# Performance work log

Hardware: AMD Instinct MI355X
Metric: run time of the kernel (lower is better)

Reference implementation:

```python
import jax, jax.numpy as jnp
import numpy as np


def setup_inputs() -> dict:
    key = jax.random.key(0)
    ks = jax.random.split(key, 6)
    T, F, INPUT_SIZE = 32768, 758, 730  # F = input_size + attributes(27) + 1(catch_ID)
    return {
        "x": jax.random.normal(ks[0], (T, F), dtype=jnp.float32),
        "weight_input": jax.random.normal(ks[1], (4, INPUT_SIZE), dtype=jnp.float32) * 0.05,
        "weight_recur": jax.random.normal(ks[2], (4, 1), dtype=jnp.float32) * 0.05,
        "bias": jax.random.normal(ks[3], (4, 1), dtype=jnp.float32) * 0.05,
        "reg_w": jax.random.normal(ks[4], (1, 1), dtype=jnp.float32),
        "reg_b": jax.random.normal(ks[5], (1,), dtype=jnp.float32),
        "h0": jnp.zeros((1,), dtype=jnp.float32),
        "c0": jnp.zeros((1,), dtype=jnp.float32),
    }


def reference(x, weight_input, weight_recur, bias, reg_w, reg_b, h0, c0):
    input_size = weight_input.shape[1]
    # x[:, :-attributes-1] in the original == first input_size columns
    x_feat = x[:, :input_size]                      # [T, input_size]
    # hoist the per-step mm(weight_input, x_t) into one GEMM: [T, 4]
    xp = x_feat @ weight_input.T
    wr = weight_recur[:, 0]                         # [4]
    b = bias[:, 0]                                  # [4]

    def step(carry, xp_t):
        h, c = carry                                # scalars (state_size == 1)
        gates = b + wr * h + xp_t                   # [4]
        f = jax.nn.sigmoid(gates[0])
        i = jax.nn.sigmoid(gates[1])
        o = jax.nn.sigmoid(gates[2])
        g = jnp.tanh(gates[3])
        c1 = f * c + i * g
        h1 = o * jnp.tanh(c1)
        return (h1, c1), (h1, c1)

    (_, _), (hs, cs) = jax.lax.scan(step, (h0[0], c0[0]), xp)
    h_n = jnp.concatenate([h0[None, :], hs[:, None]], axis=0)  # [T+1, 1]
    c_n = jnp.concatenate([c0[None, :], cs[:, None]], axis=0)  # [T+1, 1]
    q_t = (h_n @ reg_w.T + reg_b)[1:]                          # [T, 1]
    return q_t, h_n, c_n
```

## Files before the change

### kernel.cpp

```cpp
#include <hip/hip_runtime.h>

#define T_LEN 32768
#define F_DIM 758
#define IN_SZ 730
#define CHUNK_L 8
#define WARM_W 48
#define N_CHUNK (T_LEN / CHUNK_L)
#define SCAN_BLOCKS (N_CHUNK / 64)
#define STAGE_ROWS 560

#define GEMV_BLOCKS 512
#define GEMV_WAVES (GEMV_BLOCKS * 4)
#define ROWS_PER_WAVE (T_LEN / GEMV_WAVES)

__global__ __launch_bounds__(256) void gemv_gates(
    const float* __restrict__ x, const float* __restrict__ w,
    const float* __restrict__ bias, float* __restrict__ xpw) {
  const float L2E = 1.4426950408889634f;
  int lane = threadIdx.x & 63;
  int g    = lane & 3;
  int p    = lane >> 2;
  int wid  = (blockIdx.x * 256 + threadIdx.x) >> 6;

  const float* wg = w + (size_t)g * IN_SZ;
  float4 wv[12];
#pragma unroll
  for (int j = 0; j < 12; j++) {
    int c = p + 16 * j;
#pragma unroll
    for (int e = 0; e < 4; e++) {
      int k = 4 * c + e;
      ((float*)&wv[j])[e] = (k < IN_SZ) ? wg[k] : 0.f;
    }
  }
  float bg = bias[g];
  float cg = (g == 3) ? (-2.f * L2E) : (-L2E);

  const float4 z4 = {0.f, 0.f, 0.f, 0.f};
  float4 xa[12], xb[12];
  float res[ROWS_PER_WAVE];

  auto loadrow = [&](float4* dst, int row) {
    const float* xr = x + (size_t)row * F_DIM;
#pragma unroll
    for (int j = 0; j < 12; j++) {
      int c = p + 16 * j;
      dst[j] = (c < 183) ? *(const float4*)(xr + 4 * c) : z4;
    }
  };
  auto dot = [&](const float4* v) {
    float s = 0.f;
#pragma unroll
    for (int j = 0; j < 12; j++) {
      s = fmaf(v[j].x, wv[j].x, s);
      s = fmaf(v[j].y, wv[j].y, s);
      s = fmaf(v[j].z, wv[j].z, s);
      s = fmaf(v[j].w, wv[j].w, s);
    }
    s += __shfl_xor(s, 4);
    s += __shfl_xor(s, 8);
    s += __shfl_xor(s, 16);
    s += __shfl_xor(s, 32);
    return s;
  };

  loadrow(xa, wid);
  loadrow(xb, wid + GEMV_WAVES);
#pragma unroll
  for (int r = 0; r < ROWS_PER_WAVE; r += 2) {
    float sA = dot(xa);
    if (r + 2 < ROWS_PER_WAVE) loadrow(xa, wid + GEMV_WAVES * (r + 2));
    res[r] = cg * (sA + bg);
    float sB = dot(xb);
    if (r + 3 < ROWS_PER_WAVE) loadrow(xb, wid + GEMV_WAVES * (r + 3));
    res[r + 1] = cg * (sB + bg);
  }
  if (lane < 4) {
#pragma unroll
    for (int r = 0; r < ROWS_PER_WAVE; r++)
      xpw[(size_t)(wid + GEMV_WAVES * r) * 4 + lane] = res[r];
  }
}

__device__ __forceinline__ int phys(int r) {
  return (r & ~15) | ((r + (r >> 4)) & 15);
}

__global__ __launch_bounds__(64) void lstm_scan(
    const float* __restrict__ xpw, const float* __restrict__ wr,
    const float* __restrict__ rgw, const float* __restrict__ rgb,
    const float* __restrict__ h0p, const float* __restrict__ c0p,
    float* __restrict__ out) {
  const float L2E = 1.4426950408889634f;
  const float M2  = -2.f * L2E;
  __shared__ float4 lds_xp[STAGE_ROWS];
  __shared__ float  lds_h[64][CHUNK_L + 1];
  __shared__ float  lds_c[64][CHUNK_L + 1];

  int lane = threadIdx.x;
  int B0   = blockIdx.x * (64 * CHUNK_L);
  int R0   = B0 - WARM_W; if (R0 < 0) R0 = 0;

  const float4* xp4 = (const float4*)xpw;
#pragma unroll
  for (int i = 0; i < 9; i++) {
    int r = 64 * i + lane;
    if (r < STAGE_ROWS) lds_xp[phys(r)] = xp4[R0 + r];
  }
  __syncthreads();

  float w20 = -L2E * wr[0];
  float w21 = -L2E * wr[1];
  float w22 = -L2E * wr[2];
  float w23 = -2.f * L2E * wr[3];

  float h = h0p[0], c = c0p[0];

  auto stepc = [&](float4 p) {
    float u0 = fmaf(h, w20, p.x);
    float u1 = fmaf(h, w21, p.y);
    float u2 = fmaf(h, w22, p.z);
    float u3 = fmaf(h, w23, p.w);
    float f  = __builtin_amdgcn_rcpf(1.f + __builtin_amdgcn_exp2f(u0));
    float i  = __builtin_amdgcn_rcpf(1.f + __builtin_amdgcn_exp2f(u1));
    float o  = __builtin_amdgcn_rcpf(1.f + __builtin_amdgcn_exp2f(u2));
    float r3 = __builtin_amdgcn_rcpf(1.f + __builtin_amdgcn_exp2f(u3));
    c = fmaf(f, c, fmaf(2.f * i, r3, -i));
    float rt = __builtin_amdgcn_rcpf(1.f + __builtin_amdgcn_exp2f(c * M2));
    h = fmaf(2.f * o, rt, -o);
  };

  auto XP = [&](int r) {
    int rc = r < 0 ? 0 : (r > STAGE_ROWS - 1 ? STAGE_ROWS - 1 : r);
    return lds_xp[phys(rc)];
  };

  int start = B0 + lane * CHUNK_L;
  int rr = (start - WARM_W) - R0;

  float4 p0 = XP(rr), p1 = XP(rr + 1), p2 = XP(rr + 2), p3 = XP(rr + 3);

  for (int s = 0; s < WARM_W; s += 4, rr += 4) {
    float4 n0 = XP(rr + 4), n1 = XP(rr + 5), n2 = XP(rr + 6), n3 = XP(rr + 7);
    if (rr     >= 0) stepc(p0);
    if (rr + 1 >= 0) stepc(p1);
    if (rr + 2 >= 0) stepc(p2);
    if (rr + 3 >= 0) stepc(p3);
    p0 = n0; p1 = n1; p2 = n2; p3 = n3;
  }
#pragma unroll
  for (int gq = 0; gq < CHUNK_L; gq += 4, rr += 4) {
    float4 n0 = XP(rr + 4), n1 = XP(rr + 5), n2 = XP(rr + 6), n3 = XP(rr + 7);
    stepc(p0); lds_h[lane][gq + 0] = h; lds_c[lane][gq + 0] = c;
    stepc(p1); lds_h[lane][gq + 1] = h; lds_c[lane][gq + 1] = c;
    stepc(p2); lds_h[lane][gq + 2] = h; lds_c[lane][gq + 2] = c;
    stepc(p3); lds_h[lane][gq + 3] = h; lds_c[lane][gq + 3] = c;
    p0 = n0; p1 = n1; p2 = n2; p3 = n3;
  }
  __syncthreads();

  float* outq = out;
  float* outh = out + T_LEN;
  float* outc = out + 2 * T_LEN + 1;
  float rw = rgw[0], rb = rgb[0];
#pragma unroll
  for (int k = 0; k < CHUNK_L; k++) {
    int idx = lane + 64 * k;
    float hv = lds_h[idx >> 3][idx & 7];
    float cv = lds_c[idx >> 3][idx & 7];
    outq[B0 + idx]     = fmaf(hv, rw, rb);
    outh[B0 + idx + 1] = hv;
    outc[B0 + idx + 1] = cv;
  }
  if (blockIdx.x == 0 && lane == 0) { outh[0] = h0p[0]; outc[0] = c0p[0]; }
}

extern "C" void kernel_launch(void* const* d_in, const int* in_sizes, int n_in,
                              void* d_out, int out_size, void* d_ws, size_t ws_size,
                              hipStream_t stream) {
  const float* x  = (const float*)d_in[0];
  const float* wi = (const float*)d_in[1];
  const float* wr = (const float*)d_in[2];
  const float* bs = (const float*)d_in[3];
  const float* rw = (const float*)d_in[4];
  const float* rb = (const float*)d_in[5];
  const float* h0 = (const float*)d_in[6];
  const float* c0 = (const float*)d_in[7];
  float* out = (float*)d_out;
  float* xpw = (float*)d_ws;

  gemv_gates<<<GEMV_BLOCKS, 256, 0, stream>>>(x, wi, bs, xpw);
  lstm_scan<<<SCAN_BLOCKS, 64, 0, stream>>>(xpw, wr, rw, rb, h0, c0, out);
}
```

Baseline: 31.94 us.

## Stage GEMV weights in LDS and double the GEMV grid

Each block now loads the four weight rows into shared memory once, and the dot product reads them from LDS instead of keeping 48 float registers per lane. This frees registers, and the grid grows from 512 to 1024 blocks so each wave handles 8 rows instead of 16. The aim is more occupancy and memory parallelism in the bandwidth-bound GEMV. The cost is extra LDS reads inside the inner loop plus a block-level sync.

Result: slower. 32.63 us (+2.2%).

```diff
diff --git a/kernel.cpp b/kernel.cpp
--- a/kernel.cpp
+++ b/kernel.cpp
@@ -9,32 +9,41 @@
 #define SCAN_BLOCKS (N_CHUNK / 64)
 #define STAGE_ROWS 560
 
-#define GEMV_BLOCKS 512
+#define GEMV_BLOCKS 1024
 #define GEMV_WAVES (GEMV_BLOCKS * 4)
 #define ROWS_PER_WAVE (T_LEN / GEMV_WAVES)
+#define WPAD 186
 
 __global__ __launch_bounds__(256) void gemv_gates(
     const float* __restrict__ x, const float* __restrict__ w,
     const float* __restrict__ bias, float* __restrict__ xpw) {
   const float L2E = 1.4426950408889634f;
-  int lane = threadIdx.x & 63;
+  __shared__ float4 wlds[4 * WPAD];
+  int tid  = threadIdx.x;
+  int lane = tid & 63;
   int g    = lane & 3;
   int p    = lane >> 2;
-  int wid  = (blockIdx.x * 256 + threadIdx.x) >> 6;
-
-  const float* wg = w + (size_t)g * IN_SZ;
-  float4 wv[12];
-#pragma unroll
-  for (int j = 0; j < 12; j++) {
-    int c = p + 16 * j;
-#pragma unroll
-    for (int e = 0; e < 4; e++) {
-      int k = 4 * c + e;
-      ((float*)&wv[j])[e] = (k < IN_SZ) ? wg[k] : 0.f;
+  int wid  = (blockIdx.x * 256 + tid) >> 6;
+
+#pragma unroll
+  for (int m = 0; m < 3; m++) {
+    int q = tid + 256 * m;
+    if (q < 732) {
+      int gg = q / 183, cc = q - 183 * gg;
+      float4 v;
+#pragma unroll
+      for (int e = 0; e < 4; e++) {
+        int k = 4 * cc + e;
+        ((float*)&v)[e] = (k < IN_SZ) ? w[gg * IN_SZ + k] : 0.f;
+      }
+      wlds[gg * WPAD + cc] = v;
     }
   }
+  __syncthreads();
+
   float bg = bias[g];
   float cg = (g == 3) ? (-2.f * L2E) : (-L2E);
+  const float4* wb = &wlds[g * WPAD];
 
   const float4 z4 = {0.f, 0.f, 0.f, 0.f};
   float4 xa[12], xb[12];
@@ -52,10 +61,14 @@
     float s = 0.f;
 #pragma unroll
     for (int j = 0; j < 12; j++) {
-      s = fmaf(v[j].x, wv[j].x, s);
-      s = fmaf(v[j].y, wv[j].y, s);
-      s = fmaf(v[j].z, wv[j].z, s);
-      s = fmaf(v[j].w, wv[j].w, s);
+      int c = p + 16 * j;
+      if (c < 183) {
+        float4 wj = wb[c];
+        s = fmaf(v[j].x, wj.x, s);
+        s = fmaf(v[j].y, wj.y, s);
+        s = fmaf(v[j].z, wj.z, s);
+        s = fmaf(v[j].w, wj.w, s);
+      }
     }
     s += __shfl_xor(s, 4);
     s += __shfl_xor(s, 8);
```
